# Kernel tuning notes

Measured on AMD Instinct MI355X. Metric: run time of the kernel, lower is better.

Reference implementation:

```python
import jax, jax.numpy as jnp
import numpy as np

TOP_K = 8  # num_experts_per_tok
NEG_INF = -1e9


def setup_inputs() -> dict:
    key = jax.random.key(0)
    ks = jax.random.split(key, 6)
    B, S, H, I, E, G, GS = 1, 2048, 2048, 1408, 64, 8, 8
    sc = 0.02
    return {
        "hidden_states": jax.random.normal(ks[0], (B, S, H), jnp.float32),
        "gate_w": jax.random.normal(ks[1], (E, H), jnp.float32) * sc,
        "mask_up_w": jax.random.normal(ks[2], (G, H, GS), jnp.float32) * sc,
        "gate_proj_w": jax.random.normal(ks[3], (G, I, H), jnp.float32) * sc,
        "up_proj_w": jax.random.normal(ks[4], (G, I, H), jnp.float32) * sc,
        "down_proj_w": jax.random.normal(ks[5], (G, H, I), jnp.float32) * sc,
        "inv_map": jnp.arange(G * GS, dtype=jnp.int64).reshape(G, GS),
    }


def reference(hidden_states, gate_w, mask_up_w, gate_proj_w, up_proj_w, down_proj_w, inv_map):
    B, S, H = hidden_states.shape
    x = hidden_states.reshape(-1, H)  # [N, H]
    N = x.shape[0]
    E = gate_w.shape[0]

    # Gate: softmax scores -> top-k routing (DeepSeek-style MoEGate)
    scores = jax.nn.softmax(x @ gate_w.T, axis=-1)          # [N, E]
    topk_w, topk_idx = jax.lax.top_k(scores, TOP_K)         # [N, K]

    # Per-expert routing weight: w_e[t, e] = sum_k topk_w[t,k] * (topk_idx[t,k]==e)
    w_e = jnp.zeros((N, E), x.dtype).at[jnp.arange(N)[:, None], topk_idx].add(topk_w)

    # Gather group-local weights: flat[t, g, i] for sub-expert i of group g
    flat = w_e[:, inv_map]                                   # [N, G, GS]
    scalar = flat.sum(-1)                                    # [N, G]
    soft = jax.nn.softmax(jnp.where(flat == 0, NEG_INF, flat), axis=-1)  # [N, G, GS]

    # Mask injection: x' = x + mask_up_proj(soft)
    xg = x[:, None, :] + jnp.einsum('ngi,ghi->ngh', soft, mask_up_w)     # [N, G, H]

    # SwiGLU per group
    g = jnp.einsum('ngh,gih->ngi', xg, gate_proj_w)          # [N, G, I]
    u = jnp.einsum('ngh,gih->ngi', xg, up_proj_w)            # [N, G, I]
    a = jax.nn.silu(g) * u
    d = jnp.einsum('ngi,ghi->ngh', a, down_proj_w)           # [N, G, H]

    # scalar * output, accumulated over groups (scalar==0 rows contribute 0,
    # matching the original's zero-masked scatter)
    y = jnp.einsum('ng,ngh->nh', scalar, d)
    return y.reshape(B, S, H)
```

## Files before the change

kernel.cpp:

```cpp
#include <hip/hip_runtime.h>

#define N_TOK 2048
#define H_DIM 2048
#define I_DIM 1408
#define E_EXP 64
#define G_GRP 8
#define KTOT  (G_GRP * I_DIM)
#define NQ    (G_GRP * I_DIM * H_DIM / 4)
#define NQB   (NQ / 256)

typedef __bf16 bf16x8 __attribute__((ext_vector_type(8)));
typedef float f32x4 __attribute__((ext_vector_type(4)));

__device__ __forceinline__ unsigned short f2bf(float f) {
    unsigned int u = __builtin_bit_cast(unsigned int, f);
    u += 0x7fffu + ((u >> 16) & 1u);
    return (unsigned short)(u >> 16);
}

__device__ __forceinline__ void gl_lds16(const void* g, void* l) {
    __builtin_amdgcn_global_load_lds(
        (const __attribute__((address_space(1))) unsigned int*)g,
        (__attribute__((address_space(3))) unsigned int*)l, 16, 0, 0);
}

__device__ __forceinline__ bf16x8 fragP(const unsigned short* sm, int region, int row, int q) {
    int idx = region + ((row >> 1) << 3) + ((q | ((row & 1) << 2)) ^ ((row >> 1) & 7));
    return *(const bf16x8*)&sm[idx * 8];
}
__device__ __forceinline__ int slot_row(int s) {
    int line = s >> 3, u = (s & 7) ^ (line & 7);
    return (line << 1) | (u >> 2);
}
__device__ __forceinline__ int slot_q(int s) {
    int line = s >> 3, u = (s & 7) ^ (line & 7);
    return u & 3;
}

__global__ __launch_bounds__(256) void k_prep(const float* __restrict__ gw,
                                              const float* __restrict__ wgp,
                                              const float* __restrict__ wup,
                                              const float* __restrict__ wdp,
                                              float* __restrict__ gwT,
                                              unsigned short* __restrict__ wgB,
                                              unsigned short* __restrict__ wuB,
                                              unsigned short* __restrict__ wdB) {
    int b = blockIdx.x, t = threadIdx.x;
    if (b < 2 * NQB) {
        const float* in = (b < NQB) ? wgp : wup;
        unsigned short* out = (b < NQB) ? wgB : wuB;
        int i = (b < NQB ? b : b - NQB) * 256 + t;
        float4 v = ((const float4*)in)[i];
        ushort4 o;
        o.x = f2bf(v.x); o.y = f2bf(v.y); o.z = f2bf(v.z); o.w = f2bf(v.w);
        ((ushort4*)out)[i] = o;
    } else if (b < 3 * NQB) {
        int idx = (b - 2 * NQB) * 256 + t;
        int i4 = idx % (I_DIM / 4);
        int h  = (idx / (I_DIM / 4)) & (H_DIM - 1);
        int g  = idx / ((I_DIM / 4) * H_DIM);
        float4 v = ((const float4*)(wdp + ((size_t)g * H_DIM + h) * I_DIM))[i4];
        ushort4 o;
        o.x = f2bf(v.x); o.y = f2bf(v.y); o.z = f2bf(v.z); o.w = f2bf(v.w);
        ((ushort4*)(wdB + ((size_t)h * G_GRP + g) * I_DIM))[i4] = o;
    } else {
        int i = (b - 3 * NQB) * 256 + t;
        gwT[i] = gw[(i & 63) * H_DIM + (i >> 6)];
    }
}

__global__ __launch_bounds__(512) void k_gating(const float* __restrict__ x,
                                                const float* __restrict__ gwT,
                                                float* __restrict__ soft,
                                                float* __restrict__ scal) {
    __shared__ double smAcc[8][8][64];
    int t = threadIdx.x, wid = t >> 6, lane = t & 63;
    int n0 = blockIdx.x * 8;

    double acc[8];
#pragma unroll
    for (int k = 0; k < 8; ++k) acc[k] = 0.0;
    int h0 = wid * 256;
    for (int h = h0; h < h0 + 256; ++h) {
        float gv = gwT[h * 64 + lane];
#pragma unroll
        for (int tok = 0; tok < 8; ++tok)
            acc[tok] += (double)x[(size_t)(n0 + tok) * H_DIM + h] * (double)gv;
    }
#pragma unroll
    for (int tok = 0; tok < 8; ++tok) smAcc[wid][tok][lane] = acc[tok];
    __syncthreads();

    double lg = 0.0;
#pragma unroll
    for (int w2 = 0; w2 < 8; ++w2) lg += smAcc[w2][wid][lane];
    float logit = (float)lg;

    float mx = logit;
#pragma unroll
    for (int d = 1; d < 64; d <<= 1) mx = fmaxf(mx, __shfl_xor(mx, d));
    float ex = expf(logit - mx);
    float sm = ex;
#pragma unroll
    for (int d = 1; d < 64; d <<= 1) sm += __shfl_xor(sm, d);
    float prob = ex / sm;

    float cur = prob, w = 0.0f;
#pragma unroll
    for (int it = 0; it < 8; ++it) {
        float m = cur;
#pragma unroll
        for (int d = 1; d < 64; d <<= 1) m = fmaxf(m, __shfl_xor(m, d));
        unsigned long long msk = __ballot(cur == m);
        int first = __ffsll(msk) - 1;
        if (lane == first) { w = prob; cur = -1.0f; }
    }
    float wf = w;

    float s8 = wf;
#pragma unroll
    for (int d = 1; d < 8; d <<= 1) s8 += __shfl_xor(s8, d);
    float v = (wf == 0.0f) ? -1000000000.0f : wf;
    float m8 = v;
#pragma unroll
    for (int d = 1; d < 8; d <<= 1) m8 = fmaxf(m8, __shfl_xor(m8, d));
    float e8 = expf(v - m8);
    float q8 = e8;
#pragma unroll
    for (int d = 1; d < 8; d <<= 1) q8 += __shfl_xor(q8, d);

    int n = n0 + wid;
    soft[(size_t)n * 64 + lane] = e8 / q8;
    if ((lane & 7) == 0) scal[(size_t)n * 8 + (lane >> 3)] = s8;
}

__global__ __launch_bounds__(256) void k_xg(const float* __restrict__ x,
                                            const float* __restrict__ muw,
                                            const float* __restrict__ soft,
                                            unsigned short* __restrict__ xg) {
    int g = blockIdx.z, h0 = blockIdx.y * 1024, n0 = blockIdx.x * 128;
    __shared__ float smSf[128][8];
    int t = threadIdx.x;
    {
        int r = t >> 1, s4 = (t & 1) * 4;
        float4 sv = *(const float4*)&soft[(size_t)(n0 + r) * 64 + g * 8 + s4];
        smSf[r][s4 + 0] = sv.x; smSf[r][s4 + 1] = sv.y;
        smSf[r][s4 + 2] = sv.z; smSf[r][s4 + 3] = sv.w;
    }
    int hh = t * 4;
    float mu[8][4];
#pragma unroll
    for (int j = 0; j < 4; ++j) {
        const float4* p = (const float4*)(muw + ((size_t)g * H_DIM + h0 + hh + j) * 8);
        float4 a = p[0], b = p[1];
        mu[0][j] = a.x; mu[1][j] = a.y; mu[2][j] = a.z; mu[3][j] = a.w;
        mu[4][j] = b.x; mu[5][j] = b.y; mu[6][j] = b.z; mu[7][j] = b.w;
    }
    __syncthreads();
    for (int r = 0; r < 128; ++r) {
        float4 xv = *(const float4*)&x[(size_t)(n0 + r) * H_DIM + h0 + hh];
        float c0 = xv.x, c1 = xv.y, c2 = xv.z, c3 = xv.w;
#pragma unroll
        for (int s = 0; s < 8; ++s) {
            float w = smSf[r][s];
            c0 += w * mu[s][0]; c1 += w * mu[s][1];
            c2 += w * mu[s][2]; c3 += w * mu[s][3];
        }
        ushort4 o;
        o.x = f2bf(c0); o.y = f2bf(c1); o.z = f2bf(c2); o.w = f2bf(c3);
        *(ushort4*)&xg[((size_t)g * N_TOK + n0 + r) * H_DIM + h0 + hh] = o;
    }
}

#define NT_G1 (H_DIM / 32)

__global__ __launch_bounds__(512, 2) void k_gemm1(const unsigned short* __restrict__ xg,
                                                  const unsigned short* __restrict__ wg,
                                                  const unsigned short* __restrict__ wu,
                                                  const float* __restrict__ scal,
                                                  unsigned short* __restrict__ aB) {
    int f = blockIdx.x;
    int g = f & 7, r = f >> 3;
    int m0 = (r & 7) * 256;
    int n0 = (r >> 3) * 128;
    __shared__ __align__(16) unsigned short lds[4 * 2048 * 8];
    __shared__ float smS[256];
    int t = threadIdx.x, wid = t >> 6, lane = t & 63;
    int r16 = lane & 15, quad = lane >> 4;
    int wm = wid >> 2, wn = wid & 3;

    if (t < 256) smS[t] = scal[(size_t)(m0 + t) * 8 + g];

    const unsigned short* A  = xg + (size_t)g * N_TOK * H_DIM;
    const unsigned short* Bg = wg + (size_t)g * I_DIM * H_DIM;
    const unsigned short* Bu = wu + (size_t)g * I_DIM * H_DIM;

    int sA0 = (wid * 2 + 0) * 64 + lane;
    int sA1 = (wid * 2 + 1) * 64 + lane;
    int sB  = wid * 64 + lane;
    const unsigned short* gA0 = A + (size_t)(m0 + slot_row(sA0)) * H_DIM + slot_q(sA0) * 8;
    const unsigned short* gA1 = A + (size_t)(m0 + slot_row(sA1)) * H_DIM + slot_q(sA1) * 8;
    const unsigned short* gG  = Bg + (size_t)(n0 + slot_row(sB)) * H_DIM + slot_q(sB) * 8;
    const unsigned short* gU  = Bu + (size_t)(n0 + slot_row(sB)) * H_DIM + slot_q(sB) * 8;

#define STAGE_A(ts) do { int b_ = (ts) & 3; \
        gl_lds16(gA0 + (size_t)(ts) * 32, &lds[((size_t)b_ * 2048 + (wid * 2 + 0) * 64) * 8]); \
        gl_lds16(gA1 + (size_t)(ts) * 32, &lds[((size_t)b_ * 2048 + (wid * 2 + 1) * 64) * 8]); } while (0)
#define STAGE_GU(ts) do { int b_ = (ts) & 3; \
        gl_lds16(gG + (size_t)(ts) * 32, &lds[((size_t)b_ * 2048 + 1024 + wid * 64) * 8]); \
        gl_lds16(gU + (size_t)(ts) * 32, &lds[((size_t)b_ * 2048 + 1536 + wid * 64) * 8]); } while (0)

    f32x4 zero = {0.f, 0.f, 0.f, 0.f};
    f32x4 accg[8][2], accu[8][2];
#pragma unroll
    for (int mi = 0; mi < 8; ++mi)
#pragma unroll
        for (int ni = 0; ni < 2; ++ni) { accg[mi][ni] = zero; accu[mi][ni] = zero; }

    STAGE_A(0); STAGE_GU(0);
    STAGE_A(1); STAGE_GU(1);
    STAGE_A(2); STAGE_GU(2);
    asm volatile("s_waitcnt vmcnt(8) lgkmcnt(0)" ::: "memory");
    __builtin_amdgcn_s_barrier();

    for (int tt = 0; tt < NT_G1; ++tt) {
        const unsigned short* buf = &lds[(size_t)(tt & 3) * 2048 * 8];
        bf16x8 af[4], bgf[2], buf_[2];
#pragma unroll
        for (int mi = 0; mi < 4; ++mi)
            af[mi] = fragP(buf, 0, wm * 128 + mi * 16 + r16, quad);
#pragma unroll
        for (int ni = 0; ni < 2; ++ni) {
            bgf[ni]  = fragP(buf, 1024, wn * 32 + ni * 16 + r16, quad);
            buf_[ni] = fragP(buf, 1536, wn * 32 + ni * 16 + r16, quad);
        }
        if (tt + 3 < NT_G1) STAGE_A(tt + 3);
        __builtin_amdgcn_s_barrier();
        __builtin_amdgcn_s_setprio(1);
#pragma unroll
        for (int mi = 0; mi < 4; ++mi)
#pragma unroll
            for (int ni = 0; ni < 2; ++ni) {
                accg[mi][ni] = __builtin_amdgcn_mfma_f32_16x16x32_bf16(af[mi], bgf[ni], accg[mi][ni], 0, 0, 0);
                accu[mi][ni] = __builtin_amdgcn_mfma_f32_16x16x32_bf16(af[mi], buf_[ni], accu[mi][ni], 0, 0, 0);
            }
        __builtin_amdgcn_s_setprio(0);
        __builtin_amdgcn_s_barrier();
#pragma unroll
        for (int mi = 0; mi < 4; ++mi)
            af[mi] = fragP(buf, 0, wm * 128 + (mi + 4) * 16 + r16, quad);
        if (tt + 3 < NT_G1) STAGE_GU(tt + 3);
        __builtin_amdgcn_s_barrier();
        __builtin_amdgcn_s_setprio(1);
#pragma unroll
        for (int mi = 0; mi < 4; ++mi)
#pragma unroll
            for (int ni = 0; ni < 2; ++ni) {
                accg[mi + 4][ni] = __builtin_amdgcn_mfma_f32_16x16x32_bf16(af[mi], bgf[ni], accg[mi + 4][ni], 0, 0, 0);
                accu[mi + 4][ni] = __builtin_amdgcn_mfma_f32_16x16x32_bf16(af[mi], buf_[ni], accu[mi + 4][ni], 0, 0, 0);
            }
        __builtin_amdgcn_s_setprio(0);
        {
            int rem = NT_G1 - 2 - tt;
            if (rem >= 2)      asm volatile("s_waitcnt vmcnt(8)" ::: "memory");
            else if (rem == 1) asm volatile("s_waitcnt vmcnt(4)" ::: "memory");
            else if (rem == 0) asm volatile("s_waitcnt vmcnt(0)" ::: "memory");
        }
        __builtin_amdgcn_s_barrier();
    }
#undef STAGE_A
#undef STAGE_GU

#pragma unroll
    for (int mi = 0; mi < 8; ++mi)
#pragma unroll
        for (int ni = 0; ni < 2; ++ni)
#pragma unroll
            for (int rr = 0; rr < 4; ++rr) {
                int rl = wm * 128 + mi * 16 + quad * 4 + rr;
                int row = m0 + rl;
                int col = n0 + wn * 32 + ni * 16 + r16;
                float gv = accg[mi][ni][rr];
                float sv = gv / (1.0f + __expf(-gv));
                aB[((size_t)row * G_GRP + g) * I_DIM + col] = f2bf(sv * accu[mi][ni][rr] * smS[rl]);
            }
}

#define NT_G2 (KTOT / 4 / 32)

__global__ __launch_bounds__(512, 2) void k_gemm2(const unsigned short* __restrict__ aB,
                                                  const unsigned short* __restrict__ wd,
                                                  float* __restrict__ out) {
    int m0 = blockIdx.x * 256, h0 = blockIdx.y * 256;
    int kbase = blockIdx.z * (KTOT / 4);
    __shared__ __align__(16) unsigned short lds[4 * 2048 * 8];
    int t = threadIdx.x, wid = t >> 6, lane = t & 63;
    int r16 = lane & 15, quad = lane >> 4;
    int wm = wid >> 2, wn = wid & 3;

    int sA0 = (wid * 2 + 0) * 64 + lane;
    int sA1 = (wid * 2 + 1) * 64 + lane;
    const unsigned short* gA0 = aB + (size_t)(m0 + slot_row(sA0)) * KTOT + kbase + slot_q(sA0) * 8;
    const unsigned short* gA1 = aB + (size_t)(m0 + slot_row(sA1)) * KTOT + kbase + slot_q(sA1) * 8;
    const unsigned short* gB0 = wd + (size_t)(h0 + slot_row(sA0)) * KTOT + kbase + slot_q(sA0) * 8;
    const unsigned short* gB1 = wd + (size_t)(h0 + slot_row(sA1)) * KTOT + kbase + slot_q(sA1) * 8;

#define STAGE2A(ts) do { int b_ = (ts) & 3; \
        gl_lds16(gA0 + (size_t)(ts) * 32, &lds[((size_t)b_ * 2048 + (wid * 2 + 0) * 64) * 8]); \
        gl_lds16(gA1 + (size_t)(ts) * 32, &lds[((size_t)b_ * 2048 + (wid * 2 + 1) * 64) * 8]); } while (0)
#define STAGE2B(ts) do { int b_ = (ts) & 3; \
        gl_lds16(gB0 + (size_t)(ts) * 32, &lds[((size_t)b_ * 2048 + 1024 + (wid * 2 + 0) * 64) * 8]); \
        gl_lds16(gB1 + (size_t)(ts) * 32, &lds[((size_t)b_ * 2048 + 1024 + (wid * 2 + 1) * 64) * 8]); } while (0)

    f32x4 zero = {0.f, 0.f, 0.f, 0.f};
    f32x4 acc[8][4];
#pragma unroll
    for (int mi = 0; mi < 8; ++mi)
#pragma unroll
        for (int ni = 0; ni < 4; ++ni) acc[mi][ni] = zero;

    STAGE2A(0); STAGE2B(0);
    STAGE2A(1); STAGE2B(1);
    STAGE2A(2); STAGE2B(2);
    asm volatile("s_waitcnt vmcnt(8)" ::: "memory");
    __builtin_amdgcn_s_barrier();

    for (int tt = 0; tt < NT_G2; ++tt) {
        const unsigned short* buf = &lds[(size_t)(tt & 3) * 2048 * 8];
        bf16x8 af[4], bf_[4];
#pragma unroll
        for (int mi = 0; mi < 4; ++mi)
            af[mi] = fragP(buf, 0, wm * 128 + mi * 16 + r16, quad);
#pragma unroll
        for (int ni = 0; ni < 4; ++ni)
            bf_[ni] = fragP(buf, 1024, wn * 64 + ni * 16 + r16, quad);
        if (tt + 3 < NT_G2) STAGE2A(tt + 3);
        __builtin_amdgcn_s_barrier();
        __builtin_amdgcn_s_setprio(1);
#pragma unroll
        for (int mi = 0; mi < 4; ++mi)
#pragma unroll
            for (int ni = 0; ni < 4; ++ni)
                acc[mi][ni] = __builtin_amdgcn_mfma_f32_16x16x32_bf16(af[mi], bf_[ni], acc[mi][ni], 0, 0, 0);
        __builtin_amdgcn_s_setprio(0);
        __builtin_amdgcn_s_barrier();
#pragma unroll
        for (int mi = 0; mi < 4; ++mi)
            af[mi] = fragP(buf, 0, wm * 128 + (mi + 4) * 16 + r16, quad);
        if (tt + 3 < NT_G2) STAGE2B(tt + 3);
        __builtin_amdgcn_s_barrier();
        __builtin_amdgcn_s_setprio(1);
#pragma unroll
        for (int mi = 0; mi < 4; ++mi)
#pragma unroll
            for (int ni = 0; ni < 4; ++ni)
                acc[mi + 4][ni] = __builtin_amdgcn_mfma_f32_16x16x32_bf16(af[mi], bf_[ni], acc[mi + 4][ni], 0, 0, 0);
        __builtin_amdgcn_s_setprio(0);
        {
            int rem = NT_G2 - 2 - tt;
            if (rem >= 2)      asm volatile("s_waitcnt vmcnt(8)" ::: "memory");
            else if (rem == 1) asm volatile("s_waitcnt vmcnt(4)" ::: "memory");
            else if (rem == 0) asm volatile("s_waitcnt vmcnt(0)" ::: "memory");
        }
        __builtin_amdgcn_s_barrier();
    }
#undef STAGE2A
#undef STAGE2B

#pragma unroll
    for (int mi = 0; mi < 8; ++mi)
#pragma unroll
        for (int ni = 0; ni < 4; ++ni)
#pragma unroll
            for (int rr = 0; rr < 4; ++rr) {
                int row = m0 + wm * 128 + mi * 16 + quad * 4 + rr;
                int col = h0 + wn * 64 + ni * 16 + r16;
                atomicAdd(&out[(size_t)row * H_DIM + col], acc[mi][ni][rr]);
            }
}

extern "C" void kernel_launch(void* const* d_in, const int* in_sizes, int n_in,
                              void* d_out, int out_size, void* d_ws, size_t ws_size,
                              hipStream_t stream) {
    const float* x   = (const float*)d_in[0];
    const float* gw  = (const float*)d_in[1];
    const float* mu  = (const float*)d_in[2];
    const float* wgp = (const float*)d_in[3];
    const float* wup = (const float*)d_in[4];
    const float* wdp = (const float*)d_in[5];
    float* out = (float*)d_out;
    char* ws = (char*)d_ws;

    float* gwT  = (float*)(ws + 0);
    float* soft = (float*)(ws + 524288);
    float* scal = (float*)(ws + 1048576);
    unsigned short* wgB = (unsigned short*)(ws + 1114112);
    unsigned short* wuB = (unsigned short*)(ws + 47251456);
    unsigned short* wdB = (unsigned short*)(ws + 93388800);
    unsigned short* xg  = (unsigned short*)(ws + 139526144);
    unsigned short* aB  = (unsigned short*)(ws + 206635008);

    hipMemsetAsync(d_out, 0, (size_t)N_TOK * H_DIM * sizeof(float), stream);
    k_prep<<<3 * NQB + 512, 256, 0, stream>>>(gw, wgp, wup, wdp, gwT, wgB, wuB, wdB);
    k_gating<<<N_TOK / 8, 512, 0, stream>>>(x, gwT, soft, scal);
    k_xg<<<dim3(16, 2, 8), 256, 0, stream>>>(x, mu, soft, xg);
    k_gemm1<<<704, 512, 0, stream>>>(xg, wgB, wuB, scal, aB);
    k_gemm2<<<dim3(8, 8, 4), 512, 0, stream>>>(aB, wdB, out);
}
```

Measured before the change: 736.9 us.

## Software-pipeline LDS fragment reads and halve barriers in both GEMM loops

Restructures the gate/up and down-projection main loops so that the next tile's A and B fragments are read from LDS during the current tile's second MFMA half. All global-to-LDS staging for a tile is issued at the top of the iteration, and the barrier count per iteration drops from four to one. The last tile is peeled into an epilogue, and the loop is unrolled by two. This is meant to hide LDS read latency behind MFMA work and cut synchronisation overhead, at the cost of more live registers for the double-buffered fragments.

```diff
diff --git a/kernel.cpp b/kernel.cpp
--- a/kernel.cpp
+++ b/kernel.cpp
@@ -220,53 +220,83 @@
     STAGE_A(0); STAGE_GU(0);
     STAGE_A(1); STAGE_GU(1);
     STAGE_A(2); STAGE_GU(2);
-    asm volatile("s_waitcnt vmcnt(8) lgkmcnt(0)" ::: "memory");
+    asm volatile("s_waitcnt vmcnt(8)" ::: "memory");
     __builtin_amdgcn_s_barrier();
 
-    for (int tt = 0; tt < NT_G1; ++tt) {
-        const unsigned short* buf = &lds[(size_t)(tt & 3) * 2048 * 8];
-        bf16x8 af[4], bgf[2], buf_[2];
-#pragma unroll
-        for (int mi = 0; mi < 4; ++mi)
-            af[mi] = fragP(buf, 0, wm * 128 + mi * 16 + r16, quad);
-#pragma unroll
-        for (int ni = 0; ni < 2; ++ni) {
-            bgf[ni]  = fragP(buf, 1024, wn * 32 + ni * 16 + r16, quad);
-            buf_[ni] = fragP(buf, 1536, wn * 32 + ni * 16 + r16, quad);
-        }
-        if (tt + 3 < NT_G1) STAGE_A(tt + 3);
-        __builtin_amdgcn_s_barrier();
+    bf16x8 A0[4], BG[2], BU[2];
+#pragma unroll
+    for (int mi = 0; mi < 4; ++mi) A0[mi] = fragP(lds, 0, wm * 128 + mi * 16 + r16, quad);
+#pragma unroll
+    for (int ni = 0; ni < 2; ++ni) {
+        BG[ni] = fragP(lds, 1024, wn * 32 + ni * 16 + r16, quad);
+        BU[ni] = fragP(lds, 1536, wn * 32 + ni * 16 + r16, quad);
+    }
+
+#pragma unroll 2
+    for (int tt = 0; tt < NT_G1 - 1; ++tt) {
+        const unsigned short* buf  = &lds[(size_t)(tt & 3) * 2048 * 8];
+        const unsigned short* bufn = &lds[(size_t)((tt + 1) & 3) * 2048 * 8];
+        if (tt + 3 < NT_G1) { STAGE_A(tt + 3); STAGE_GU(tt + 3); }
+        bf16x8 A1[4];
+#pragma unroll
+        for (int mi = 0; mi < 4; ++mi) A1[mi] = fragP(buf, 0, wm * 128 + (mi + 4) * 16 + r16, quad);
         __builtin_amdgcn_s_setprio(1);
 #pragma unroll
         for (int mi = 0; mi < 4; ++mi)
 #pragma unroll
             for (int ni = 0; ni < 2; ++ni) {
-                accg[mi][ni] = __builtin_amdgcn_mfma_f32_16x16x32_bf16(af[mi], bgf[ni], accg[mi][ni], 0, 0, 0);
-                accu[mi][ni] = __builtin_amdgcn_mfma_f32_16x16x32_bf16(af[mi], buf_[ni], accu[mi][ni], 0, 0, 0);
-            }
-        __builtin_amdgcn_s_setprio(0);
-        __builtin_amdgcn_s_barrier();
-#pragma unroll
-        for (int mi = 0; mi < 4; ++mi)
-            af[mi] = fragP(buf, 0, wm * 128 + (mi + 4) * 16 + r16, quad);
-        if (tt + 3 < NT_G1) STAGE_GU(tt + 3);
-        __builtin_amdgcn_s_barrier();
-        __builtin_amdgcn_s_setprio(1);
-#pragma unroll
-        for (int mi = 0; mi < 4; ++mi)
-#pragma unroll
-            for (int ni = 0; ni < 2; ++ni) {
-                accg[mi + 4][ni] = __builtin_amdgcn_mfma_f32_16x16x32_bf16(af[mi], bgf[ni], accg[mi + 4][ni], 0, 0, 0);
-                accu[mi + 4][ni] = __builtin_amdgcn_mfma_f32_16x16x32_bf16(af[mi], buf_[ni], accu[mi + 4][ni], 0, 0, 0);
+                accg[mi][ni] = __builtin_amdgcn_mfma_f32_16x16x32_bf16(A0[mi], BG[ni], accg[mi][ni], 0, 0, 0);
+                accu[mi][ni] = __builtin_amdgcn_mfma_f32_16x16x32_bf16(A0[mi], BU[ni], accu[mi][ni], 0, 0, 0);
             }
         __builtin_amdgcn_s_setprio(0);
         {
-            int rem = NT_G1 - 2 - tt;
-            if (rem >= 2)      asm volatile("s_waitcnt vmcnt(8)" ::: "memory");
-            else if (rem == 1) asm volatile("s_waitcnt vmcnt(4)" ::: "memory");
-            else if (rem == 0) asm volatile("s_waitcnt vmcnt(0)" ::: "memory");
+            int rem = NT_G1 - 1 - tt;
+            if (rem >= 3)      asm volatile("s_waitcnt vmcnt(8)" ::: "memory");
+            else if (rem == 2) asm volatile("s_waitcnt vmcnt(4)" ::: "memory");
+            else               asm volatile("s_waitcnt vmcnt(0)" ::: "memory");
         }
         __builtin_amdgcn_s_barrier();
+        bf16x8 nA0[4], nBG[2], nBU[2];
+#pragma unroll
+        for (int mi = 0; mi < 4; ++mi) nA0[mi] = fragP(bufn, 0, wm * 128 + mi * 16 + r16, quad);
+#pragma unroll
+        for (int ni = 0; ni < 2; ++ni) {
+            nBG[ni] = fragP(bufn, 1024, wn * 32 + ni * 16 + r16, quad);
+            nBU[ni] = fragP(bufn, 1536, wn * 32 + ni * 16 + r16, quad);
+        }
+        __builtin_amdgcn_s_setprio(1);
+#pragma unroll
+        for (int mi = 0; mi < 4; ++mi)
+#pragma unroll
+            for (int ni = 0; ni < 2; ++ni) {
+                accg[mi + 4][ni] = __builtin_amdgcn_mfma_f32_16x16x32_bf16(A1[mi], BG[ni], accg[mi + 4][ni], 0, 0, 0);
+                accu[mi + 4][ni] = __builtin_amdgcn_mfma_f32_16x16x32_bf16(A1[mi], BU[ni], accu[mi + 4][ni], 0, 0, 0);
+            }
+        __builtin_amdgcn_s_setprio(0);
+#pragma unroll
+        for (int mi = 0; mi < 4; ++mi) A0[mi] = nA0[mi];
+#pragma unroll
+        for (int ni = 0; ni < 2; ++ni) { BG[ni] = nBG[ni]; BU[ni] = nBU[ni]; }
+    }
+    {
+        const unsigned short* buf = &lds[(size_t)((NT_G1 - 1) & 3) * 2048 * 8];
+        bf16x8 A1[4];
+#pragma unroll
+        for (int mi = 0; mi < 4; ++mi) A1[mi] = fragP(buf, 0, wm * 128 + (mi + 4) * 16 + r16, quad);
+#pragma unroll
+        for (int mi = 0; mi < 4; ++mi)
+#pragma unroll
+            for (int ni = 0; ni < 2; ++ni) {
+                accg[mi][ni] = __builtin_amdgcn_mfma_f32_16x16x32_bf16(A0[mi], BG[ni], accg[mi][ni], 0, 0, 0);
+                accu[mi][ni] = __builtin_amdgcn_mfma_f32_16x16x32_bf16(A0[mi], BU[ni], accu[mi][ni], 0, 0, 0);
+            }
+#pragma unroll
+        for (int mi = 0; mi < 4; ++mi)
+#pragma unroll
+            for (int ni = 0; ni < 2; ++ni) {
+                accg[mi + 4][ni] = __builtin_amdgcn_mfma_f32_16x16x32_bf16(A1[mi], BG[ni], accg[mi + 4][ni], 0, 0, 0);
+                accu[mi + 4][ni] = __builtin_amdgcn_mfma_f32_16x16x32_bf16(A1[mi], BU[ni], accu[mi + 4][ni], 0, 0, 0);
+            }
     }
 #undef STAGE_A
 #undef STAGE_GU
@@ -325,44 +355,66 @@
     asm volatile("s_waitcnt vmcnt(8)" ::: "memory");
     __builtin_amdgcn_s_barrier();
 
-    for (int tt = 0; tt < NT_G2; ++tt) {
-        const unsigned short* buf = &lds[(size_t)(tt & 3) * 2048 * 8];
-        bf16x8 af[4], bf_[4];
-#pragma unroll
-        for (int mi = 0; mi < 4; ++mi)
-            af[mi] = fragP(buf, 0, wm * 128 + mi * 16 + r16, quad);
-#pragma unroll
-        for (int ni = 0; ni < 4; ++ni)
-            bf_[ni] = fragP(buf, 1024, wn * 64 + ni * 16 + r16, quad);
-        if (tt + 3 < NT_G2) STAGE2A(tt + 3);
-        __builtin_amdgcn_s_barrier();
+    bf16x8 A0[4], BB[4];
+#pragma unroll
+    for (int mi = 0; mi < 4; ++mi) A0[mi] = fragP(lds, 0, wm * 128 + mi * 16 + r16, quad);
+#pragma unroll
+    for (int ni = 0; ni < 4; ++ni) BB[ni] = fragP(lds, 1024, wn * 64 + ni * 16 + r16, quad);
+
+#pragma unroll 2
+    for (int tt = 0; tt < NT_G2 - 1; ++tt) {
+        const unsigned short* buf  = &lds[(size_t)(tt & 3) * 2048 * 8];
+        const unsigned short* bufn = &lds[(size_t)((tt + 1) & 3) * 2048 * 8];
+        if (tt + 3 < NT_G2) { STAGE2A(tt + 3); STAGE2B(tt + 3); }
+        bf16x8 A1[4];
+#pragma unroll
+        for (int mi = 0; mi < 4; ++mi) A1[mi] = fragP(buf, 0, wm * 128 + (mi + 4) * 16 + r16, quad);
         __builtin_amdgcn_s_setprio(1);
 #pragma unroll
         for (int mi = 0; mi < 4; ++mi)
 #pragma unroll
             for (int ni = 0; ni < 4; ++ni)
-                acc[mi][ni] = __builtin_amdgcn_mfma_f32_16x16x32_bf16(af[mi], bf_[ni], acc[mi][ni], 0, 0, 0);
-        __builtin_amdgcn_s_setprio(0);
-        __builtin_amdgcn_s_barrier();
-#pragma unroll
-        for (int mi = 0; mi < 4; ++mi)
-            af[mi] = fragP(buf, 0, wm * 128 + (mi + 4) * 16 + r16, quad);
-        if (tt + 3 < NT_G2) STAGE2B(tt + 3);
-        __builtin_amdgcn_s_barrier();
-        __builtin_amdgcn_s_setprio(1);
-#pragma unroll
-        for (int mi = 0; mi < 4; ++mi)
-#pragma unroll
-            for (int ni = 0; ni < 4; ++ni)
-                acc[mi + 4][ni] = __builtin_amdgcn_mfma_f32_16x16x32_bf16(af[mi], bf_[ni], acc[mi + 4][ni], 0, 0, 0);
+                acc[mi][ni] = __builtin_amdgcn_mfma_f32_16x16x32_bf16(A0[mi], BB[ni], acc[mi][ni], 0, 0, 0);
         __builtin_amdgcn_s_setprio(0);
         {
-            int rem = NT_G2 - 2 - tt;
-            if (rem >= 2)      asm volatile("s_waitcnt vmcnt(8)" ::: "memory");
-            else if (rem == 1) asm volatile("s_waitcnt vmcnt(4)" ::: "memory");
-            else if (rem == 0) asm volatile("s_waitcnt vmcnt(0)" ::: "memory");
+            int rem = NT_G2 - 1 - tt;
+            if (rem >= 3)      asm volatile("s_waitcnt vmcnt(8)" ::: "memory");
+            else if (rem == 2) asm volatile("s_waitcnt vmcnt(4)" ::: "memory");
+            else               asm volatile("s_waitcnt vmcnt(0)" ::: "memory");
         }
         __builtin_amdgcn_s_barrier();
+        bf16x8 nA0[4], nBB[4];
+#pragma unroll
+        for (int mi = 0; mi < 4; ++mi) nA0[mi] = fragP(bufn, 0, wm * 128 + mi * 16 + r16, quad);
+#pragma unroll
+        for (int ni = 0; ni < 4; ++ni) nBB[ni] = fragP(bufn, 1024, wn * 64 + ni * 16 + r16, quad);
+        __builtin_amdgcn_s_setprio(1);
+#pragma unroll
+        for (int mi = 0; mi < 4; ++mi)
+#pragma unroll
+            for (int ni = 0; ni < 4; ++ni)
+                acc[mi + 4][ni] = __builtin_amdgcn_mfma_f32_16x16x32_bf16(A1[mi], BB[ni], acc[mi + 4][ni], 0, 0, 0);
+        __builtin_amdgcn_s_setprio(0);
+#pragma unroll
+        for (int mi = 0; mi < 4; ++mi) A0[mi] = nA0[mi];
+#pragma unroll
+        for (int ni = 0; ni < 4; ++ni) BB[ni] = nBB[ni];
+    }
+    {
+        const unsigned short* buf = &lds[(size_t)((NT_G2 - 1) & 3) * 2048 * 8];
+        bf16x8 A1[4];
+#pragma unroll
+        for (int mi = 0; mi < 4; ++mi) A1[mi] = fragP(buf, 0, wm * 128 + (mi + 4) * 16 + r16, quad);
+#pragma unroll
+        for (int mi = 0; mi < 4; ++mi)
+#pragma unroll
+            for (int ni = 0; ni < 4; ++ni)
+                acc[mi][ni] = __builtin_amdgcn_mfma_f32_16x16x32_bf16(A0[mi], BB[ni], acc[mi][ni], 0, 0, 0);
+#pragma unroll
+        for (int mi = 0; mi < 4; ++mi)
+#pragma unroll
+            for (int ni = 0; ni < 4; ++ni)
+                acc[mi + 4][ni] = __builtin_amdgcn_mfma_f32_16x16x32_bf16(A1[mi], BB[ni], acc[mi + 4][ni], 0, 0, 0);
     }
 #undef STAGE2A
 #undef STAGE2B
```

Result: faster. 702.9 us (-4.6%).
